# Optimization experiments

Measured on AMD Instinct MI355X. Metric: run time of the kernel, lower is better.

## Reference

```python
import jax, jax.numpy as jnp
import numpy as np

B = 65536      # batch
D = 512        # embedding_dim
H = 256        # hidden_size
NB = 6         # num_branch


def setup_inputs() -> dict:
    key = jax.random.key(0)
    ks = jax.random.split(key, 12)
    sc = 0.05
    s = lambda k, shape: (jax.random.normal(k, shape, jnp.float32) * sc)
    inp = {}
    inp["embedding"] = jax.random.normal(ks[0], (B, D), jnp.float32)
    inp["speed"] = jax.random.normal(ks[1], (B,), jnp.float32)
    inp["command"] = jax.random.randint(ks[2], (B,), 1, NB + 1)  # values 1..6
    # speed_in: Linear(1,H) -> ReLU -> Linear(H,D)   (weights stored [in,out])
    inp["sw1"] = s(ks[3], (1, H)); inp["sb1"] = jnp.zeros((H,), jnp.float32)
    inp["sw2"] = s(ks[4], (H, D)); inp["sb2"] = jnp.zeros((D,), jnp.float32)
    # 6 branch MLPs, stacked along leading axis: D->H->H->3, sigmoid
    inp["bw1"] = s(ks[5], (NB, D, H)); inp["bb1"] = jnp.zeros((NB, H), jnp.float32)
    inp["bw2"] = s(ks[6], (NB, H, H)); inp["bb2"] = jnp.zeros((NB, H), jnp.float32)
    inp["bw3"] = s(ks[7], (NB, H, 3)); inp["bb3"] = jnp.zeros((NB, 3), jnp.float32)
    # speed_out: D->H->H->1
    inp["ow1"] = s(ks[8], (D, H)); inp["ob1"] = jnp.zeros((H,), jnp.float32)
    inp["ow2"] = s(ks[9], (H, H)); inp["ob2"] = jnp.zeros((H,), jnp.float32)
    inp["ow3"] = s(ks[10], (H, 1)); inp["ob3"] = jnp.zeros((1,), jnp.float32)
    return inp


def reference(embedding, speed, command,
              sw1, sb1, sw2, sb2,
              bw1, bb1, bw2, bb2, bw3, bb3,
              ow1, ob1, ow2, ob2, ow3, ob3):
    # embedding += speed_in(speed.unsqueeze(1))
    sh = jax.nn.relu(speed[:, None] @ sw1 + sb1)           # [B,H]
    emb = embedding + (sh @ sw2 + sb2)                      # [B,D]

    # all 6 branches computed densely (as in the original), then masked
    h = jax.nn.relu(jnp.einsum('bd,ndh->nbh', emb, bw1) + bb1[:, None, :])   # [NB,B,H]
    h = jax.nn.relu(jnp.einsum('nbh,nhk->nbk', h, bw2) + bb2[:, None, :])    # [NB,B,H]
    br = jax.nn.sigmoid(jnp.einsum('nbh,nho->nbo', h, bw3) + bb3[:, None, :])  # [NB,B,3]

    # mask: branch i selected where i == command - 1
    mask = (jnp.arange(NB)[:, None] == (command - 1)[None, :]).astype(br.dtype)  # [NB,B]
    control_pred = jnp.sum(br * mask[:, :, None], axis=0)   # [B,3]

    # speed_out head
    t = jax.nn.relu(emb @ ow1 + ob1)
    t = jax.nn.relu(t @ ow2 + ob2)
    speed_pred = t @ ow3 + ob3                               # [B,1]
    return control_pred, speed_pred
```

## Files before the change

### kernel.cpp

```cpp
#include <hip/hip_runtime.h>
#include <math.h>


#define B_ 65536
#define D_ 512
#define H_ 256

typedef float  f32x4   __attribute__((ext_vector_type(4)));
typedef __bf16 bf16x8  __attribute__((ext_vector_type(8)));
typedef __bf16 bf16x4  __attribute__((ext_vector_type(4)));
typedef float  float4v __attribute__((ext_vector_type(4)));

#define OFF_CURSORS  64
#define OFF_PERM     256
#define OFF_PACK     262400
#define WS_NEEDED    3277056

#define PKO_SW2   0u
#define PKO_BW1   131072u
#define PKO_BW2   917504u
#define PKO_OW1   1310720u
#define PKO_OW2   1441792u

#define PITCH_E 520


__global__ __launch_bounds__(1024) void k_countscan(const int* __restrict__ command,
                                                    int* __restrict__ cursors) {
    __shared__ int red[6][1024];
    int t = threadIdx.x;
    int cnt[6] = {0, 0, 0, 0, 0, 0};
    const int4* c4p = (const int4*)command;
    for (int i = t; i < B_ / 4; i += 1024) {
        int4 v = c4p[i];
        int a[4] = {v.x, v.y, v.z, v.w};
        #pragma unroll
        for (int j = 0; j < 4; ++j) {
            int c = min(max(a[j] - 1, 0), 5);
            #pragma unroll
            for (int k = 0; k < 6; ++k) cnt[k] += (c == k);
        }
    }
    #pragma unroll
    for (int k = 0; k < 6; ++k) red[k][t] = cnt[k];
    __syncthreads();
    for (int s = 512; s > 0; s >>= 1) {
        if (t < s) {
            #pragma unroll
            for (int c = 0; c < 6; ++c) red[c][t] += red[c][t + s];
        }
        __syncthreads();
    }
    if (t == 0) {
        int sum = 0;
        #pragma unroll
        for (int c = 0; c < 6; ++c) { cursors[c] = sum; sum += red[c][0]; }
    }
}


__global__ __launch_bounds__(256) void k_prepB(const int* __restrict__ command,
                                               int* __restrict__ cursors,
                                               int* __restrict__ perm,
                                               const float* __restrict__ sw2,
                                               const float* __restrict__ bw1,
                                               const float* __restrict__ bw2,
                                               const float* __restrict__ ow1,
                                               const float* __restrict__ ow2,
                                               __bf16* __restrict__ PK) {
    int t = threadIdx.x;
    if (blockIdx.x < 256) {
        __shared__ int lh[6], lbase[6];
        if (t < 6) lh[t] = 0;
        __syncthreads();
        int i = blockIdx.x * 256 + t;
        int c = command[i] - 1; c = min(max(c, 0), 5);
        int rank = atomicAdd(&lh[c], 1);
        __syncthreads();
        if (t < 6) lbase[t] = atomicAdd(&cursors[t], lh[t]);
        __syncthreads();
        perm[lbase[c] + rank] = i;
        return;
    }
    int b = blockIdx.x - 256;
    const float* src; int srcN, colOff; unsigned dstOff; int tt;
    if (b < 64)       { int s = b >> 5;        tt = b & 31;  src = sw2;                          srcN = 512; colOff = s * 256; dstOff = PKO_SW2 + s * 65536u; }
    else if (b < 448) { int i = b - 64;  int c = i >> 6; tt = i & 63; src = bw1 + (size_t)c * 512 * 256; srcN = 256; colOff = 0; dstOff = PKO_BW1 + c * 131072u; }
    else if (b < 640) { int i = b - 448; int c = i >> 5; tt = i & 31; src = bw2 + (size_t)c * 256 * 256; srcN = 256; colOff = 0; dstOff = PKO_BW2 + c * 65536u; }
    else if (b < 704) { tt = b - 640; src = ow1; srcN = 256; colOff = 0; dstOff = PKO_OW1; }
    else              { tt = b - 704; src = ow2; srcN = 256; colOff = 0; dstOff = PKO_OW2; }
    int kc = tt >> 2, nt = tt & 3;
    int k0 = kc * 32, n0 = nt * 64;

    __shared__ __bf16 T[64][34];
    #pragma unroll
    for (int p = 0; p < 8; ++p) {
        int idx = p * 256 + t;
        int k = idx >> 6, n = idx & 63;
        T[n][k] = (__bf16)src[(size_t)(k0 + k) * srcN + colOff + n0 + n];
    }
    __syncthreads();
    int n = t >> 2, seg = t & 3;
    bf16x8 v;
    #pragma unroll
    for (int j = 0; j < 8; ++j) v[j] = T[n][seg * 8 + j];
    *(bf16x8*)(PK + dstOff + ((unsigned)(kc * 256 + n0 + n) * 32u + seg * 8u)) = v;
}


__global__ __launch_bounds__(256, 4) void k_fused(
    const float* __restrict__ embedding, const float* __restrict__ speed,
    const int*   __restrict__ command,
    const float* __restrict__ sw1, const float* __restrict__ sb1,
    const float* __restrict__ sb2,
    const float* __restrict__ bb1, const float* __restrict__ bb2,
    const float* __restrict__ bw3, const float* __restrict__ bb3,
    const float* __restrict__ ob1, const float* __restrict__ ob2,
    const float* __restrict__ ow3, const float* __restrict__ ob3,
    const int* __restrict__ perm, const __bf16* __restrict__ PK,
    float* __restrict__ out)
{
    __shared__ __bf16 s_x[32 * PITCH_E];
    __shared__ float  s_head[32][4];
    __shared__ int    s_row[32];
    __shared__ int    s_cmd[32];
    __shared__ float  s_spd[32];

    const int tid = threadIdx.x;
    const int w = tid >> 6, lane = tid & 63;
    const int lm = lane & 15, kg = lane >> 4;
    const int R0 = blockIdx.x * 32;

    if (tid < 32) {
        int r = perm[R0 + tid];
        s_row[tid] = r;
        int c = command[r] - 1; c = min(max(c, 0), 5);
        s_cmd[tid] = c;
        s_spd[tid] = speed[r];
        s_head[tid][0] = 0.f; s_head[tid][1] = 0.f; s_head[tid][2] = 0.f; s_head[tid][3] = 0.f;
    }
    __syncthreads();

    #pragma unroll
    for (int it = 0; it < 16; ++it) {
        int idx = it * 256 + tid;
        int row = idx >> 7, c4 = idx & 127;
        float4v v = __builtin_nontemporal_load(
            (const float4v*)(embedding + (size_t)s_row[row] * D_ + c4 * 4));
        bf16x4 pv;
        pv[0] = (__bf16)v[0]; pv[1] = (__bf16)v[1];
        pv[2] = (__bf16)v[2]; pv[3] = (__bf16)v[3];
        *(bf16x4*)(s_x + row * PITCH_E + c4 * 4) = pv;
    }
    __syncthreads();

    int cc[2][4];
    #pragma unroll
    for (int mt = 0; mt < 2; ++mt)
        #pragma unroll
        for (int g = 0; g < 4; ++g)
            cc[mt][g] = s_cmd[mt * 16 + kg * 4 + g];

    int myc = s_cmd[lane & 31];
    int cmin = myc, cmax = myc;
    #pragma unroll
    for (int d = 1; d < 32; d <<= 1) {
        cmin = min(cmin, __shfl_xor(cmin, d));
        cmax = max(cmax, __shfl_xor(cmax, d));
    }

    {
        const float spd0 = s_spd[lm], spd1 = s_spd[16 + lm];
        const unsigned slice = (unsigned)(w >> 1) * 65536u;
        const int mbase = (w & 1) * 128;
        f32x4 dacc[8][2];
        #pragma unroll
        for (int mt = 0; mt < 8; ++mt) {
            dacc[mt][0] = f32x4{0.f, 0.f, 0.f, 0.f};
            dacc[mt][1] = f32x4{0.f, 0.f, 0.f, 0.f};
        }
        #pragma unroll 2
        for (int ks = 0; ks < 8; ++ks) {
            const int k0 = ks * 32 + kg * 8;
            float4v w0 = *(const float4v*)(sw1 + k0);
            float4v w1 = *(const float4v*)(sw1 + k0 + 4);
            float4v c0 = *(const float4v*)(sb1 + k0);
            float4v c1 = *(const float4v*)(sb1 + k0 + 4);
            bf16x8 b0, b1;
            #pragma unroll
            for (int j = 0; j < 4; ++j) {
                b0[j]     = (__bf16)fmaxf(spd0 * w0[j] + c0[j], 0.f);
                b0[j + 4] = (__bf16)fmaxf(spd0 * w1[j] + c1[j], 0.f);
                b1[j]     = (__bf16)fmaxf(spd1 * w0[j] + c0[j], 0.f);
                b1[j + 4] = (__bf16)fmaxf(spd1 * w1[j] + c1[j], 0.f);
            }
            const __bf16* ap = PK + PKO_SW2 + slice + (size_t)ks * 8192
                             + (size_t)(mbase + lm) * 32 + kg * 8;
            #pragma unroll
            for (int mt = 0; mt < 8; ++mt) {
                bf16x8 av = *(const bf16x8*)(ap + mt * 512);
                dacc[mt][0] = __builtin_amdgcn_mfma_f32_16x16x32_bf16(av, b0, dacc[mt][0], 0, 0, 0);
                dacc[mt][1] = __builtin_amdgcn_mfma_f32_16x16x32_bf16(av, b1, dacc[mt][1], 0, 0, 0);
            }
        }
        #pragma unroll
        for (int mt = 0; mt < 8; ++mt) {
            int colb = w * 128 + mt * 16 + kg * 4;
            float4v sbv = *(const float4v*)(sb2 + colb);
            #pragma unroll
            for (int nt = 0; nt < 2; ++nt) {
                int row = nt * 16 + lm;
                bf16x4* p = (bf16x4*)(s_x + row * PITCH_E + colb);
                bf16x4 old = *p;
                bf16x4 nv;
                #pragma unroll
                for (int g = 0; g < 4; ++g)
                    nv[g] = (__bf16)(dacc[mt][nt][g] + sbv[g] + (float)old[g]);
                *p = nv;
            }
        }
    }
    __syncthreads();

    const int wq = w & 1;
    const bool roleB = (w < 2);
    const __bf16* aX0 = s_x + lm * PITCH_E + kg * 8;
    const __bf16* aX1 = aX0 + 16 * PITCH_E;
    const unsigned laneoff = (unsigned)(wq * 128 + lm) * 32u + kg * 8u;

    bf16x4 res[2][8];
    if (roleB) {
        for (int c = cmin; c <= cmax; ++c) {
            const __bf16* bb = PK + PKO_BW1 + c * 131072u + laneoff;
            #pragma unroll
            for (int half = 0; half < 2; ++half) {
                f32x4 ah[2][4];
                #pragma unroll
                for (int mt = 0; mt < 2; ++mt)
                    #pragma unroll
                    for (int ct = 0; ct < 4; ++ct) ah[mt][ct] = f32x4{0.f, 0.f, 0.f, 0.f};
                const __bf16* bp = bb + half * 2048;
                #pragma unroll 2
                for (int ks = 0; ks < 16; ++ks) {
                    bf16x8 a0 = *(const bf16x8*)(aX0 + ks * 32);
                    bf16x8 a1 = *(const bf16x8*)(aX1 + ks * 32);
                    #pragma unroll
                    for (int ct = 0; ct < 4; ++ct) {
                        bf16x8 bv = *(const bf16x8*)(bp + (size_t)ks * 8192 + ct * 512);
                        ah[0][ct] = __builtin_amdgcn_mfma_f32_16x16x32_bf16(a0, bv, ah[0][ct], 0, 0, 0);
                        ah[1][ct] = __builtin_amdgcn_mfma_f32_16x16x32_bf16(a1, bv, ah[1][ct], 0, 0, 0);
                    }
                }
                #pragma unroll
                for (int ct = 0; ct < 4; ++ct) {
                    int col = wq * 128 + (half * 4 + ct) * 16 + lm;
                    float b = bb1[c * H_ + col];
                    #pragma unroll
                    for (int mt = 0; mt < 2; ++mt)
                        #pragma unroll
                        for (int g = 0; g < 4; ++g)
                            if (cc[mt][g] == c)
                                res[mt][half * 4 + ct][g] = (__bf16)fmaxf(ah[mt][ct][g] + b, 0.f);
                }
            }
        }
    } else {
        const __bf16* bb = PK + PKO_OW1 + laneoff;
        #pragma unroll
        for (int half = 0; half < 2; ++half) {
            f32x4 ta[2][4];
            #pragma unroll
            for (int mt = 0; mt < 2; ++mt)
                #pragma unroll
                for (int ct = 0; ct < 4; ++ct) ta[mt][ct] = f32x4{0.f, 0.f, 0.f, 0.f};
            const __bf16* bp = bb + half * 2048;
            #pragma unroll 2
            for (int ks = 0; ks < 16; ++ks) {
                bf16x8 a0 = *(const bf16x8*)(aX0 + ks * 32);
                bf16x8 a1 = *(const bf16x8*)(aX1 + ks * 32);
                #pragma unroll
                for (int ct = 0; ct < 4; ++ct) {
                    bf16x8 bv = *(const bf16x8*)(bp + (size_t)ks * 8192 + ct * 512);
                    ta[0][ct] = __builtin_amdgcn_mfma_f32_16x16x32_bf16(a0, bv, ta[0][ct], 0, 0, 0);
                    ta[1][ct] = __builtin_amdgcn_mfma_f32_16x16x32_bf16(a1, bv, ta[1][ct], 0, 0, 0);
                }
            }
            #pragma unroll
            for (int ct = 0; ct < 4; ++ct) {
                int col = wq * 128 + (half * 4 + ct) * 16 + lm;
                float b = ob1[col];
                #pragma unroll
                for (int mt = 0; mt < 2; ++mt)
                    #pragma unroll
                    for (int g = 0; g < 4; ++g)
                        res[mt][half * 4 + ct][g] = (__bf16)fmaxf(ta[mt][ct][g] + b, 0.f);
            }
        }
    }
    __syncthreads();

    {
        const int colBase = (roleB ? 0 : 256) + wq * 128;
        #pragma unroll
        for (int ct = 0; ct < 8; ++ct) {
            int col = colBase + ct * 16 + lm;
            #pragma unroll
            for (int mt = 0; mt < 2; ++mt)
                #pragma unroll
                for (int g = 0; g < 4; ++g)
                    s_x[(mt * 16 + kg * 4 + g) * PITCH_E + col] = res[mt][ct][g];
        }
    }
    __syncthreads();

    const __bf16* aH0 = s_x + lm * PITCH_E + (roleB ? 0 : 256) + kg * 8;
    const __bf16* aH1 = aH0 + 16 * PITCH_E;
    if (roleB) {
        for (int c = cmin; c <= cmax; ++c) {
            float ph[2][4][3];
            #pragma unroll
            for (int mt = 0; mt < 2; ++mt)
                #pragma unroll
                for (int g = 0; g < 4; ++g) { ph[mt][g][0] = 0.f; ph[mt][g][1] = 0.f; ph[mt][g][2] = 0.f; }
            const __bf16* bb = PK + PKO_BW2 + c * 65536u + laneoff;
            #pragma unroll
            for (int half = 0; half < 2; ++half) {
                f32x4 hh[2][4];
                #pragma unroll
                for (int mt = 0; mt < 2; ++mt)
                    #pragma unroll
                    for (int ct = 0; ct < 4; ++ct) hh[mt][ct] = f32x4{0.f, 0.f, 0.f, 0.f};
                const __bf16* bp = bb + half * 2048;
                #pragma unroll 2
                for (int ks = 0; ks < 8; ++ks) {
                    bf16x8 a0 = *(const bf16x8*)(aH0 + ks * 32);
                    bf16x8 a1 = *(const bf16x8*)(aH1 + ks * 32);
                    #pragma unroll
                    for (int ct = 0; ct < 4; ++ct) {
                        bf16x8 bv = *(const bf16x8*)(bp + (size_t)ks * 8192 + ct * 512);
                        hh[0][ct] = __builtin_amdgcn_mfma_f32_16x16x32_bf16(a0, bv, hh[0][ct], 0, 0, 0);
                        hh[1][ct] = __builtin_amdgcn_mfma_f32_16x16x32_bf16(a1, bv, hh[1][ct], 0, 0, 0);
                    }
                }
                #pragma unroll
                for (int ct = 0; ct < 4; ++ct) {
                    int col = wq * 128 + (half * 4 + ct) * 16 + lm;
                    float b  = bb2[c * H_ + col];
                    float w0 = bw3[(c * H_ + col) * 3 + 0];
                    float w1 = bw3[(c * H_ + col) * 3 + 1];
                    float w2 = bw3[(c * H_ + col) * 3 + 2];
                    #pragma unroll
                    for (int mt = 0; mt < 2; ++mt)
                        #pragma unroll
                        for (int g = 0; g < 4; ++g) {
                            float h = fmaxf(hh[mt][ct][g] + b, 0.f);
                            ph[mt][g][0] += h * w0; ph[mt][g][1] += h * w1; ph[mt][g][2] += h * w2;
                        }
                }
            }
            #pragma unroll
            for (int mt = 0; mt < 2; ++mt)
                #pragma unroll
                for (int g = 0; g < 4; ++g)
                    #pragma unroll
                    for (int o = 0; o < 3; ++o) {
                        float v = ph[mt][g][o];
                        v += __shfl_xor(v, 1); v += __shfl_xor(v, 2);
                        v += __shfl_xor(v, 4); v += __shfl_xor(v, 8);
                        ph[mt][g][o] = v;
                    }
            if (lm == 0) {
                #pragma unroll
                for (int mt = 0; mt < 2; ++mt)
                    #pragma unroll
                    for (int g = 0; g < 4; ++g)
                        if (cc[mt][g] == c) {
                            int row = mt * 16 + kg * 4 + g;
                            atomicAdd(&s_head[row][0], ph[mt][g][0]);
                            atomicAdd(&s_head[row][1], ph[mt][g][1]);
                            atomicAdd(&s_head[row][2], ph[mt][g][2]);
                        }
            }
        }
    } else {
        float sp[2][4];
        #pragma unroll
        for (int mt = 0; mt < 2; ++mt)
            #pragma unroll
            for (int g = 0; g < 4; ++g) sp[mt][g] = 0.f;
        const __bf16* bb = PK + PKO_OW2 + laneoff;
        #pragma unroll
        for (int half = 0; half < 2; ++half) {
            f32x4 hh[2][4];
            #pragma unroll
            for (int mt = 0; mt < 2; ++mt)
                #pragma unroll
                for (int ct = 0; ct < 4; ++ct) hh[mt][ct] = f32x4{0.f, 0.f, 0.f, 0.f};
            const __bf16* bp = bb + half * 2048;
            #pragma unroll 2
            for (int ks = 0; ks < 8; ++ks) {
                bf16x8 a0 = *(const bf16x8*)(aH0 + ks * 32);
                bf16x8 a1 = *(const bf16x8*)(aH1 + ks * 32);
                #pragma unroll
                for (int ct = 0; ct < 4; ++ct) {
                    bf16x8 bv = *(const bf16x8*)(bp + (size_t)ks * 8192 + ct * 512);
                    hh[0][ct] = __builtin_amdgcn_mfma_f32_16x16x32_bf16(a0, bv, hh[0][ct], 0, 0, 0);
                    hh[1][ct] = __builtin_amdgcn_mfma_f32_16x16x32_bf16(a1, bv, hh[1][ct], 0, 0, 0);
                }
            }
            #pragma unroll
            for (int ct = 0; ct < 4; ++ct) {
                int col = wq * 128 + (half * 4 + ct) * 16 + lm;
                float b = ob2[col], wv = ow3[col];
                #pragma unroll
                for (int mt = 0; mt < 2; ++mt)
                    #pragma unroll
                    for (int g = 0; g < 4; ++g)
                        sp[mt][g] += fmaxf(hh[mt][ct][g] + b, 0.f) * wv;
            }
        }
        #pragma unroll
        for (int mt = 0; mt < 2; ++mt)
            #pragma unroll
            for (int g = 0; g < 4; ++g) {
                float v = sp[mt][g];
                v += __shfl_xor(v, 1); v += __shfl_xor(v, 2);
                v += __shfl_xor(v, 4); v += __shfl_xor(v, 8);
                if (lm == 0) atomicAdd(&s_head[mt * 16 + kg * 4 + g][3], v);
            }
    }
    __syncthreads();

    if (tid < 32) {
        int r = s_row[tid], c = s_cmd[tid];
        #pragma unroll
        for (int o = 0; o < 3; ++o) {
            float x = s_head[tid][o] + bb3[c * 3 + o];
            __builtin_nontemporal_store(1.f / (1.f + __expf(-x)), &out[(size_t)r * 3 + o]);
        }
        __builtin_nontemporal_store(s_head[tid][3] + ob3[0], &out[(size_t)3 * B_ + r]);
    }
}


__global__ __launch_bounds__(256) void cilrs_slow(
    const float* __restrict__ embedding, const float* __restrict__ speed,
    const int* __restrict__ command,
    const float* __restrict__ sw1, const float* __restrict__ sb1,
    const float* __restrict__ sw2, const float* __restrict__ sb2,
    const float* __restrict__ bw1, const float* __restrict__ bb1,
    const float* __restrict__ bw2, const float* __restrict__ bb2,
    const float* __restrict__ bw3, const float* __restrict__ bb3,
    const float* __restrict__ ow1, const float* __restrict__ ob1,
    const float* __restrict__ ow2, const float* __restrict__ ob2,
    const float* __restrict__ ow3, const float* __restrict__ ob3,
    float* __restrict__ out)
{
    const int row = blockIdx.x;
    const int j   = threadIdx.x;
    __shared__ float sh[H_];
    __shared__ float emb[D_];
    __shared__ float h1[H_];
    __shared__ float h2[H_];
    const float spd = speed[row];
    { float v = spd * sw1[j] + sb1[j]; sh[j] = v > 0.f ? v : 0.f; }
    __syncthreads();
    {
        float a0 = 0.f, a1 = 0.f;
        for (int h = 0; h < H_; ++h) {
            const float s = sh[h];
            a0 += s * sw2[h * D_ + j];
            a1 += s * sw2[h * D_ + j + 256];
        }
        emb[j]       = embedding[(size_t)row * D_ + j]       + a0 + sb2[j];
        emb[j + 256] = embedding[(size_t)row * D_ + j + 256] + a1 + sb2[j + 256];
    }
    __syncthreads();
    const int n = command[row] - 1;
    {
        const float* wp = bw1 + (size_t)n * D_ * H_;
        float a = 0.f;
        for (int d = 0; d < D_; ++d) a += emb[d] * wp[d * H_ + j];
        a += bb1[n * H_ + j];
        h1[j] = a > 0.f ? a : 0.f;
    }
    __syncthreads();
    {
        const float* wp = bw2 + (size_t)n * H_ * H_;
        float a = 0.f;
        for (int h = 0; h < H_; ++h) a += h1[h] * wp[h * H_ + j];
        a += bb2[n * H_ + j];
        h2[j] = a > 0.f ? a : 0.f;
    }
    __syncthreads();
    {
        float a = 0.f;
        for (int d = 0; d < D_; ++d) a += emb[d] * ow1[d * H_ + j];
        a += ob1[j];
        sh[j] = a > 0.f ? a : 0.f;
    }
    __syncthreads();
    {
        float a = 0.f;
        for (int h = 0; h < H_; ++h) a += sh[h] * ow2[h * H_ + j];
        a += ob2[j];
        h1[j] = a > 0.f ? a : 0.f;
    }
    __syncthreads();
    if (j < 3) {
        const float* wp = bw3 + (size_t)n * H_ * 3;
        float a = 0.f;
        for (int h = 0; h < H_; ++h) a += h2[h] * wp[h * 3 + j];
        a += bb3[n * 3 + j];
        out[(size_t)row * 3 + j] = 1.f / (1.f + expf(-a));
    } else if (j == 3) {
        float a = 0.f;
        for (int h = 0; h < H_; ++h) a += h1[h] * ow3[h];
        a += ob3[0];
        out[(size_t)B_ * 3 + row] = a;
    }
}


extern "C" void kernel_launch(void* const* d_in, const int* in_sizes, int n_in,
                              void* d_out, int out_size, void* d_ws, size_t ws_size,
                              hipStream_t stream) {
    const float* embedding = (const float*)d_in[0];
    const float* speed     = (const float*)d_in[1];
    const int*   command   = (const int*)  d_in[2];
    const float* sw1 = (const float*)d_in[3];
    const float* sb1 = (const float*)d_in[4];
    const float* sw2 = (const float*)d_in[5];
    const float* sb2 = (const float*)d_in[6];
    const float* bw1 = (const float*)d_in[7];
    const float* bb1 = (const float*)d_in[8];
    const float* bw2 = (const float*)d_in[9];
    const float* bb2 = (const float*)d_in[10];
    const float* bw3 = (const float*)d_in[11];
    const float* bb3 = (const float*)d_in[12];
    const float* ow1 = (const float*)d_in[13];
    const float* ob1 = (const float*)d_in[14];
    const float* ow2 = (const float*)d_in[15];
    const float* ob2 = (const float*)d_in[16];
    const float* ow3 = (const float*)d_in[17];
    const float* ob3 = (const float*)d_in[18];
    float* out = (float*)d_out;

    if (ws_size < (size_t)WS_NEEDED) {
        cilrs_slow<<<B_, 256, 0, stream>>>(embedding, speed, command,
                                           sw1, sb1, sw2, sb2,
                                           bw1, bb1, bw2, bb2, bw3, bb3,
                                           ow1, ob1, ow2, ob2, ow3, ob3, out);
        return;
    }

    char* ws = (char*)d_ws;
    int*    cursors = (int*)   (ws + OFF_CURSORS);
    int*    perm    = (int*)   (ws + OFF_PERM);
    __bf16* PK      = (__bf16*)(ws + OFF_PACK);

    k_countscan<<<1, 1024, 0, stream>>>(command, cursors);
    k_prepB<<<992, 256, 0, stream>>>(command, cursors, perm,
                                     sw2, bw1, bw2, ow1, ow2, PK);
    k_fused<<<B_ / 32, 256, 0, stream>>>(embedding, speed, command,
                                         sw1, sb1, sb2,
                                         bb1, bb2, bw3, bb3,
                                         ob1, ob2, ow3, ob3,
                                         perm, PK, out);
}
```

Measured before the change: 415.2 us.

## Double fused kernel row tile to 64 rows with 512-thread blocks

The fused MLP kernel now handles 64 sorted rows per block with 8 waves instead of 32 rows with 4 waves, so each wave computes a 64x64 output tile. Each packed bf16 weight fragment loaded from global memory now feeds twice as many MFMA ops, which cuts weight re-reads across blocks. The branch range is read from the first and last sorted row instead of a shuffle reduction. Separately, the weight-pack kernel switches to float4 loads, and the embedding gather drops the nontemporal hint. In exchange, per-block LDS roughly doubles and register pressure rises sharply; the launch bound of 512 threads with 4 blocks may force the compiler to spill.

```diff
diff --git a/kernel.cpp b/kernel.cpp
--- a/kernel.cpp
+++ b/kernel.cpp
@@ -94,10 +94,14 @@
 
     __shared__ __bf16 T[64][34];
     #pragma unroll
-    for (int p = 0; p < 8; ++p) {
+    for (int p = 0; p < 2; ++p) {
         int idx = p * 256 + t;
-        int k = idx >> 6, n = idx & 63;
-        T[n][k] = (__bf16)src[(size_t)(k0 + k) * srcN + colOff + n0 + n];
+        int k = idx >> 4, n4 = idx & 15;
+        float4v v = *(const float4v*)(src + (size_t)(k0 + k) * srcN + colOff + n0 + n4 * 4);
+        T[n4 * 4 + 0][k] = (__bf16)v[0];
+        T[n4 * 4 + 1][k] = (__bf16)v[1];
+        T[n4 * 4 + 2][k] = (__bf16)v[2];
+        T[n4 * 4 + 3][k] = (__bf16)v[3];
     }
     __syncthreads();
     int n = t >> 2, seg = t & 3;
@@ -108,7 +112,7 @@
 }
 
 
-__global__ __launch_bounds__(256, 4) void k_fused(
+__global__ __launch_bounds__(512, 4) void k_fused(
     const float* __restrict__ embedding, const float* __restrict__ speed,
     const int*   __restrict__ command,
     const float* __restrict__ sw1, const float* __restrict__ sb1,
@@ -120,18 +124,18 @@
     const int* __restrict__ perm, const __bf16* __restrict__ PK,
     float* __restrict__ out)
 {
-    __shared__ __bf16 s_x[32 * PITCH_E];
-    __shared__ float  s_head[32][4];
-    __shared__ int    s_row[32];
-    __shared__ int    s_cmd[32];
-    __shared__ float  s_spd[32];
+    __shared__ __bf16 s_x[64 * PITCH_E];
+    __shared__ float  s_head[64][4];
+    __shared__ int    s_row[64];
+    __shared__ int    s_cmd[64];
+    __shared__ float  s_spd[64];
 
     const int tid = threadIdx.x;
     const int w = tid >> 6, lane = tid & 63;
     const int lm = lane & 15, kg = lane >> 4;
-    const int R0 = blockIdx.x * 32;
-
-    if (tid < 32) {
+    const int R0 = blockIdx.x * 64;
+
+    if (tid < 64) {
         int r = perm[R0 + tid];
         s_row[tid] = r;
         int c = command[r] - 1; c = min(max(c, 0), 5);
@@ -143,10 +147,9 @@
 
     #pragma unroll
     for (int it = 0; it < 16; ++it) {
-        int idx = it * 256 + tid;
+        int idx = it * 512 + tid;
         int row = idx >> 7, c4 = idx & 127;
-        float4v v = __builtin_nontemporal_load(
-            (const float4v*)(embedding + (size_t)s_row[row] * D_ + c4 * 4));
+        float4v v = *(const float4v*)(embedding + (size_t)s_row[row] * D_ + c4 * 4);
         bf16x4 pv;
         pv[0] = (__bf16)v[0]; pv[1] = (__bf16)v[1];
         pv[2] = (__bf16)v[2]; pv[3] = (__bf16)v[3];
@@ -154,31 +157,19 @@
     }
     __syncthreads();
 
-    int cc[2][4];
-    #pragma unroll
-    for (int mt = 0; mt < 2; ++mt)
-        #pragma unroll
-        for (int g = 0; g < 4; ++g)
-            cc[mt][g] = s_cmd[mt * 16 + kg * 4 + g];
-
-    int myc = s_cmd[lane & 31];
-    int cmin = myc, cmax = myc;
-    #pragma unroll
-    for (int d = 1; d < 32; d <<= 1) {
-        cmin = min(cmin, __shfl_xor(cmin, d));
-        cmax = max(cmax, __shfl_xor(cmax, d));
-    }
-
-    {
-        const float spd0 = s_spd[lm], spd1 = s_spd[16 + lm];
-        const unsigned slice = (unsigned)(w >> 1) * 65536u;
-        const int mbase = (w & 1) * 128;
-        f32x4 dacc[8][2];
-        #pragma unroll
-        for (int mt = 0; mt < 8; ++mt) {
-            dacc[mt][0] = f32x4{0.f, 0.f, 0.f, 0.f};
-            dacc[mt][1] = f32x4{0.f, 0.f, 0.f, 0.f};
-        }
+    const int cmin = s_cmd[0], cmax = s_cmd[63];
+
+    {
+        float spd[4];
+        #pragma unroll
+        for (int nt = 0; nt < 4; ++nt) spd[nt] = s_spd[nt * 16 + lm];
+        const unsigned slice = (unsigned)(w >> 2) * 65536u;
+        const int mbase = (w & 3) * 64;
+        f32x4 dacc[4][4];
+        #pragma unroll
+        for (int mt = 0; mt < 4; ++mt)
+            #pragma unroll
+            for (int nt = 0; nt < 4; ++nt) dacc[mt][nt] = f32x4{0.f, 0.f, 0.f, 0.f};
         #pragma unroll 2
         for (int ks = 0; ks < 8; ++ks) {
             const int k0 = ks * 32 + kg * 8;
@@ -186,29 +177,30 @@
             float4v w1 = *(const float4v*)(sw1 + k0 + 4);
             float4v c0 = *(const float4v*)(sb1 + k0);
             float4v c1 = *(const float4v*)(sb1 + k0 + 4);
-            bf16x8 b0, b1;
-            #pragma unroll
-            for (int j = 0; j < 4; ++j) {
-                b0[j]     = (__bf16)fmaxf(spd0 * w0[j] + c0[j], 0.f);
-                b0[j + 4] = (__bf16)fmaxf(spd0 * w1[j] + c1[j], 0.f);
-                b1[j]     = (__bf16)fmaxf(spd1 * w0[j] + c0[j], 0.f);
-                b1[j + 4] = (__bf16)fmaxf(spd1 * w1[j] + c1[j], 0.f);
-            }
+            bf16x8 bns[4];
+            #pragma unroll
+            for (int nt = 0; nt < 4; ++nt)
+                #pragma unroll
+                for (int j = 0; j < 4; ++j) {
+                    bns[nt][j]     = (__bf16)fmaxf(spd[nt] * w0[j] + c0[j], 0.f);
+                    bns[nt][j + 4] = (__bf16)fmaxf(spd[nt] * w1[j] + c1[j], 0.f);
+                }
             const __bf16* ap = PK + PKO_SW2 + slice + (size_t)ks * 8192
                              + (size_t)(mbase + lm) * 32 + kg * 8;
             #pragma unroll
-            for (int mt = 0; mt < 8; ++mt) {
+            for (int mt = 0; mt < 4; ++mt) {
                 bf16x8 av = *(const bf16x8*)(ap + mt * 512);
-                dacc[mt][0] = __builtin_amdgcn_mfma_f32_16x16x32_bf16(av, b0, dacc[mt][0], 0, 0, 0);
-                dacc[mt][1] = __builtin_amdgcn_mfma_f32_16x16x32_bf16(av, b1, dacc[mt][1], 0, 0, 0);
-            }
-        }
-        #pragma unroll
-        for (int mt = 0; mt < 8; ++mt) {
-            int colb = w * 128 + mt * 16 + kg * 4;
+                #pragma unroll
+                for (int nt = 0; nt < 4; ++nt)
+                    dacc[mt][nt] = __builtin_amdgcn_mfma_f32_16x16x32_bf16(av, bns[nt], dacc[mt][nt], 0, 0, 0);
+            }
+        }
+        #pragma unroll
+        for (int mt = 0; mt < 4; ++mt) {
+            int colb = w * 64 + mt * 16 + kg * 4;
             float4v sbv = *(const float4v*)(sb2 + colb);
             #pragma unroll
-            for (int nt = 0; nt < 2; ++nt) {
+            for (int nt = 0; nt < 4; ++nt) {
                 int row = nt * 16 + lm;
                 bf16x4* p = (bf16x4*)(s_x + row * PITCH_E + colb);
                 bf16x4 old = *p;
@@ -222,90 +214,87 @@
     }
     __syncthreads();
 
-    const int wq = w & 1;
-    const bool roleB = (w < 2);
-    const __bf16* aX0 = s_x + lm * PITCH_E + kg * 8;
-    const __bf16* aX1 = aX0 + 16 * PITCH_E;
-    const unsigned laneoff = (unsigned)(wq * 128 + lm) * 32u + kg * 8u;
-
-    bf16x4 res[2][8];
+    const bool roleB = (w < 4);
+    const int colbase = (w & 3) * 64;
+    const unsigned laneoffB = (unsigned)(colbase + lm) * 32u + kg * 8u;
+    const __bf16* aXbase = s_x + lm * PITCH_E + kg * 8;
+
+    bf16x4 res[4][4];
     if (roleB) {
         for (int c = cmin; c <= cmax; ++c) {
-            const __bf16* bb = PK + PKO_BW1 + c * 131072u + laneoff;
-            #pragma unroll
-            for (int half = 0; half < 2; ++half) {
-                f32x4 ah[2][4];
-                #pragma unroll
-                for (int mt = 0; mt < 2; ++mt)
-                    #pragma unroll
-                    for (int ct = 0; ct < 4; ++ct) ah[mt][ct] = f32x4{0.f, 0.f, 0.f, 0.f};
-                const __bf16* bp = bb + half * 2048;
-                #pragma unroll 2
-                for (int ks = 0; ks < 16; ++ks) {
-                    bf16x8 a0 = *(const bf16x8*)(aX0 + ks * 32);
-                    bf16x8 a1 = *(const bf16x8*)(aX1 + ks * 32);
-                    #pragma unroll
-                    for (int ct = 0; ct < 4; ++ct) {
-                        bf16x8 bv = *(const bf16x8*)(bp + (size_t)ks * 8192 + ct * 512);
-                        ah[0][ct] = __builtin_amdgcn_mfma_f32_16x16x32_bf16(a0, bv, ah[0][ct], 0, 0, 0);
-                        ah[1][ct] = __builtin_amdgcn_mfma_f32_16x16x32_bf16(a1, bv, ah[1][ct], 0, 0, 0);
-                    }
-                }
-                #pragma unroll
-                for (int ct = 0; ct < 4; ++ct) {
-                    int col = wq * 128 + (half * 4 + ct) * 16 + lm;
-                    float b = bb1[c * H_ + col];
-                    #pragma unroll
-                    for (int mt = 0; mt < 2; ++mt)
-                        #pragma unroll
-                        for (int g = 0; g < 4; ++g)
-                            if (cc[mt][g] == c)
-                                res[mt][half * 4 + ct][g] = (__bf16)fmaxf(ah[mt][ct][g] + b, 0.f);
-                }
-            }
-        }
-    } else {
-        const __bf16* bb = PK + PKO_OW1 + laneoff;
-        #pragma unroll
-        for (int half = 0; half < 2; ++half) {
-            f32x4 ta[2][4];
-            #pragma unroll
-            for (int mt = 0; mt < 2; ++mt)
-                #pragma unroll
-                for (int ct = 0; ct < 4; ++ct) ta[mt][ct] = f32x4{0.f, 0.f, 0.f, 0.f};
-            const __bf16* bp = bb + half * 2048;
+            const __bf16* bb = PK + PKO_BW1 + (unsigned)c * 131072u + laneoffB;
+            f32x4 ah[4][4];
+            #pragma unroll
+            for (int mt = 0; mt < 4; ++mt)
+                #pragma unroll
+                for (int ct = 0; ct < 4; ++ct) ah[mt][ct] = f32x4{0.f, 0.f, 0.f, 0.f};
             #pragma unroll 2
             for (int ks = 0; ks < 16; ++ks) {
-                bf16x8 a0 = *(const bf16x8*)(aX0 + ks * 32);
-                bf16x8 a1 = *(const bf16x8*)(aX1 + ks * 32);
+                bf16x8 a[4];
+                #pragma unroll
+                for (int mt = 0; mt < 4; ++mt)
+                    a[mt] = *(const bf16x8*)(aXbase + mt * 16 * PITCH_E + ks * 32);
                 #pragma unroll
                 for (int ct = 0; ct < 4; ++ct) {
-                    bf16x8 bv = *(const bf16x8*)(bp + (size_t)ks * 8192 + ct * 512);
-                    ta[0][ct] = __builtin_amdgcn_mfma_f32_16x16x32_bf16(a0, bv, ta[0][ct], 0, 0, 0);
-                    ta[1][ct] = __builtin_amdgcn_mfma_f32_16x16x32_bf16(a1, bv, ta[1][ct], 0, 0, 0);
+                    bf16x8 bv = *(const bf16x8*)(bb + (size_t)ks * 8192 + ct * 512);
+                    #pragma unroll
+                    for (int mt = 0; mt < 4; ++mt)
+                        ah[mt][ct] = __builtin_amdgcn_mfma_f32_16x16x32_bf16(a[mt], bv, ah[mt][ct], 0, 0, 0);
                 }
             }
             #pragma unroll
             for (int ct = 0; ct < 4; ++ct) {
-                int col = wq * 128 + (half * 4 + ct) * 16 + lm;
-                float b = ob1[col];
-                #pragma unroll
-                for (int mt = 0; mt < 2; ++mt)
+                int col = colbase + ct * 16 + lm;
+                float b = bb1[c * H_ + col];
+                #pragma unroll
+                for (int mt = 0; mt < 4; ++mt)
                     #pragma unroll
                     for (int g = 0; g < 4; ++g)
-                        res[mt][half * 4 + ct][g] = (__bf16)fmaxf(ta[mt][ct][g] + b, 0.f);
-            }
-        }
-    }
-    __syncthreads();
-
-    {
-        const int colBase = (roleB ? 0 : 256) + wq * 128;
-        #pragma unroll
-        for (int ct = 0; ct < 8; ++ct) {
-            int col = colBase + ct * 16 + lm;
-            #pragma unroll
-            for (int mt = 0; mt < 2; ++mt)
+                        if (s_cmd[mt * 16 + kg * 4 + g] == c)
+                            res[mt][ct][g] = (__bf16)fmaxf(ah[mt][ct][g] + b, 0.f);
+            }
+        }
+    } else {
+        const __bf16* bb = PK + PKO_OW1 + laneoffB;
+        f32x4 ta[4][4];
+        #pragma unroll
+        for (int mt = 0; mt < 4; ++mt)
+            #pragma unroll
+            for (int ct = 0; ct < 4; ++ct) ta[mt][ct] = f32x4{0.f, 0.f, 0.f, 0.f};
+        #pragma unroll 2
+        for (int ks = 0; ks < 16; ++ks) {
+            bf16x8 a[4];
+            #pragma unroll
+            for (int mt = 0; mt < 4; ++mt)
+                a[mt] = *(const bf16x8*)(aXbase + mt * 16 * PITCH_E + ks * 32);
+            #pragma unroll
+            for (int ct = 0; ct < 4; ++ct) {
+                bf16x8 bv = *(const bf16x8*)(bb + (size_t)ks * 8192 + ct * 512);
+                #pragma unroll
+                for (int mt = 0; mt < 4; ++mt)
+                    ta[mt][ct] = __builtin_amdgcn_mfma_f32_16x16x32_bf16(a[mt], bv, ta[mt][ct], 0, 0, 0);
+            }
+        }
+        #pragma unroll
+        for (int ct = 0; ct < 4; ++ct) {
+            int col = colbase + ct * 16 + lm;
+            float b = ob1[col];
+            #pragma unroll
+            for (int mt = 0; mt < 4; ++mt)
+                #pragma unroll
+                for (int g = 0; g < 4; ++g)
+                    res[mt][ct][g] = (__bf16)fmaxf(ta[mt][ct][g] + b, 0.f);
+        }
+    }
+    __syncthreads();
+
+    {
+        const int colW = (roleB ? 0 : 256) + colbase;
+        #pragma unroll
+        for (int ct = 0; ct < 4; ++ct) {
+            int col = colW + ct * 16 + lm;
+            #pragma unroll
+            for (int mt = 0; mt < 4; ++mt)
                 #pragma unroll
                 for (int g = 0; g < 4; ++g)
                     s_x[(mt * 16 + kg * 4 + g) * PITCH_E + col] = res[mt][ct][g];
@@ -313,38 +302,36 @@
     }
     __syncthreads();
 
-    const __bf16* aH0 = s_x + lm * PITCH_E + (roleB ? 0 : 256) + kg * 8;
-    const __bf16* aH1 = aH0 + 16 * PITCH_E;
+    const __bf16* aHbase = s_x + lm * PITCH_E + (roleB ? 0 : 256) + kg * 8;
     if (roleB) {
         for (int c = cmin; c <= cmax; ++c) {
-            float ph[2][4][3];
-            #pragma unroll
-            for (int mt = 0; mt < 2; ++mt)
-                #pragma unroll
-                for (int g = 0; g < 4; ++g) { ph[mt][g][0] = 0.f; ph[mt][g][1] = 0.f; ph[mt][g][2] = 0.f; }
-            const __bf16* bb = PK + PKO_BW2 + c * 65536u + laneoff;
-            #pragma unroll
-            for (int half = 0; half < 2; ++half) {
+            const __bf16* bb = PK + PKO_BW2 + (unsigned)c * 65536u + laneoffB;
+            #pragma unroll
+            for (int rh = 0; rh < 2; ++rh) {
                 f32x4 hh[2][4];
                 #pragma unroll
                 for (int mt = 0; mt < 2; ++mt)
                     #pragma unroll
                     for (int ct = 0; ct < 4; ++ct) hh[mt][ct] = f32x4{0.f, 0.f, 0.f, 0.f};
-                const __bf16* bp = bb + half * 2048;
                 #pragma unroll 2
                 for (int ks = 0; ks < 8; ++ks) {
-                    bf16x8 a0 = *(const bf16x8*)(aH0 + ks * 32);
-                    bf16x8 a1 = *(const bf16x8*)(aH1 + ks * 32);
+                    bf16x8 a0 = *(const bf16x8*)(aHbase + (rh * 2 + 0) * 16 * PITCH_E + ks * 32);
+                    bf16x8 a1 = *(const bf16x8*)(aHbase + (rh * 2 + 1) * 16 * PITCH_E + ks * 32);
                     #pragma unroll
                     for (int ct = 0; ct < 4; ++ct) {
-                        bf16x8 bv = *(const bf16x8*)(bp + (size_t)ks * 8192 + ct * 512);
+                        bf16x8 bv = *(const bf16x8*)(bb + (size_t)ks * 8192 + ct * 512);
                         hh[0][ct] = __builtin_amdgcn_mfma_f32_16x16x32_bf16(a0, bv, hh[0][ct], 0, 0, 0);
                         hh[1][ct] = __builtin_amdgcn_mfma_f32_16x16x32_bf16(a1, bv, hh[1][ct], 0, 0, 0);
                     }
                 }
+                float ph[2][4][3];
+                #pragma unroll
+                for (int mt = 0; mt < 2; ++mt)
+                    #pragma unroll
+                    for (int g = 0; g < 4; ++g) { ph[mt][g][0] = 0.f; ph[mt][g][1] = 0.f; ph[mt][g][2] = 0.f; }
                 #pragma unroll
                 for (int ct = 0; ct < 4; ++ct) {
-                    int col = wq * 128 + (half * 4 + ct) * 16 + lm;
+                    int col = colbase + ct * 16 + lm;
                     float b  = bb2[c * H_ + col];
                     float w0 = bw3[(c * H_ + col) * 3 + 0];
                     float w1 = bw3[(c * H_ + col) * 3 + 1];
@@ -357,70 +344,70 @@
                             ph[mt][g][0] += h * w0; ph[mt][g][1] += h * w1; ph[mt][g][2] += h * w2;
                         }
                 }
-            }
+                #pragma unroll
+                for (int mt = 0; mt < 2; ++mt)
+                    #pragma unroll
+                    for (int g = 0; g < 4; ++g)
+                        #pragma unroll
+                        for (int o = 0; o < 3; ++o) {
+                            float v = ph[mt][g][o];
+                            v += __shfl_xor(v, 1); v += __shfl_xor(v, 2);
+                            v += __shfl_xor(v, 4); v += __shfl_xor(v, 8);
+                            ph[mt][g][o] = v;
+                        }
+                if (lm == 0) {
+                    #pragma unroll
+                    for (int mt = 0; mt < 2; ++mt)
+                        #pragma unroll
+                        for (int g = 0; g < 4; ++g) {
+                            int row = (rh * 2 + mt) * 16 + kg * 4 + g;
+                            if (s_cmd[row] == c) {
+                                atomicAdd(&s_head[row][0], ph[mt][g][0]);
+                                atomicAdd(&s_head[row][1], ph[mt][g][1]);
+                                atomicAdd(&s_head[row][2], ph[mt][g][2]);
+                            }
+                        }
+                }
+            }
+        }
+    } else {
+        float sp[4][4];
+        #pragma unroll
+        for (int mt = 0; mt < 4; ++mt)
+            #pragma unroll
+            for (int g = 0; g < 4; ++g) sp[mt][g] = 0.f;
+        const __bf16* bb = PK + PKO_OW2 + laneoffB;
+        #pragma unroll
+        for (int rh = 0; rh < 2; ++rh) {
+            f32x4 hh[2][4];
             #pragma unroll
             for (int mt = 0; mt < 2; ++mt)
                 #pragma unroll
-                for (int g = 0; g < 4; ++g)
-                    #pragma unroll
-                    for (int o = 0; o < 3; ++o) {
-                        float v = ph[mt][g][o];
-                        v += __shfl_xor(v, 1); v += __shfl_xor(v, 2);
-                        v += __shfl_xor(v, 4); v += __shfl_xor(v, 8);
-                        ph[mt][g][o] = v;
-                    }
-            if (lm == 0) {
-                #pragma unroll
-                for (int mt = 0; mt < 2; ++mt)
-                    #pragma unroll
-                    for (int g = 0; g < 4; ++g)
-                        if (cc[mt][g] == c) {
-                            int row = mt * 16 + kg * 4 + g;
-                            atomicAdd(&s_head[row][0], ph[mt][g][0]);
-                            atomicAdd(&s_head[row][1], ph[mt][g][1]);
-                            atomicAdd(&s_head[row][2], ph[mt][g][2]);
-                        }
-            }
-        }
-    } else {
-        float sp[2][4];
-        #pragma unroll
-        for (int mt = 0; mt < 2; ++mt)
-            #pragma unroll
-            for (int g = 0; g < 4; ++g) sp[mt][g] = 0.f;
-        const __bf16* bb = PK + PKO_OW2 + laneoff;
-        #pragma unroll
-        for (int half = 0; half < 2; ++half) {
-            f32x4 hh[2][4];
-            #pragma unroll
-            for (int mt = 0; mt < 2; ++mt)
-                #pragma unroll
                 for (int ct = 0; ct < 4; ++ct) hh[mt][ct] = f32x4{0.f, 0.f, 0.f, 0.f};
-            const __bf16* bp = bb + half * 2048;
             #pragma unroll 2
             for (int ks = 0; ks < 8; ++ks) {
-                bf16x8 a0 = *(const bf16x8*)(aH0 + ks * 32);
-                bf16x8 a1 = *(const bf16x8*)(aH1 + ks * 32);
+                bf16x8 a0 = *(const bf16x8*)(aHbase + (rh * 2 + 0) * 16 * PITCH_E + ks * 32);
+                bf16x8 a1 = *(const bf16x8*)(aHbase + (rh * 2 + 1) * 16 * PITCH_E + ks * 32);
                 #pragma unroll
                 for (int ct = 0; ct < 4; ++ct) {
-                    bf16x8 bv = *(const bf16x8*)(bp + (size_t)ks * 8192 + ct * 512);
+                    bf16x8 bv = *(const bf16x8*)(bb + (size_t)ks * 8192 + ct * 512);
                     hh[0][ct] = __builtin_amdgcn_mfma_f32_16x16x32_bf16(a0, bv, hh[0][ct], 0, 0, 0);
                     hh[1][ct] = __builtin_amdgcn_mfma_f32_16x16x32_bf16(a1, bv, hh[1][ct], 0, 0, 0);
                 }
             }
             #pragma unroll
             for (int ct = 0; ct < 4; ++ct) {
-                int col = wq * 128 + (half * 4 + ct) * 16 + lm;
+                int col = colbase + ct * 16 + lm;
                 float b = ob2[col], wv = ow3[col];
                 #pragma unroll
                 for (int mt = 0; mt < 2; ++mt)
                     #pragma unroll
                     for (int g = 0; g < 4; ++g)
-                        sp[mt][g] += fmaxf(hh[mt][ct][g] + b, 0.f) * wv;
-            }
-        }
-        #pragma unroll
-        for (int mt = 0; mt < 2; ++mt)
+                        sp[rh * 2 + mt][g] += fmaxf(hh[mt][ct][g] + b, 0.f) * wv;
+            }
+        }
+        #pragma unroll
+        for (int mt = 0; mt < 4; ++mt)
             #pragma unroll
             for (int g = 0; g < 4; ++g) {
                 float v = sp[mt][g];
@@ -431,7 +418,7 @@
     }
     __syncthreads();
 
-    if (tid < 32) {
+    if (tid < 64) {
         int r = s_row[tid], c = s_cmd[tid];
         #pragma unroll
         for (int o = 0; o < 3; ++o) {
@@ -562,7 +549,7 @@
     k_countscan<<<1, 1024, 0, stream>>>(command, cursors);
     k_prepB<<<992, 256, 0, stream>>>(command, cursors, perm,
                                      sw2, bw1, bw2, ow1, ow2, PK);
-    k_fused<<<B_ / 32, 256, 0, stream>>>(embedding, speed, command,
+    k_fused<<<B_ / 64, 512, 0, stream>>>(embedding, speed, command,
                                          sw1, sb1, sb2,
                                          bb1, bb2, bw3, bb3,
                                          ob1, ob2, ow3, ob3,
```

Result: faster. 376.0 us (-9.5%).
